# Kernel optimization log

Hardware: AMD Instinct MI355X
Metric: run time of the kernel (lower is better)

Reference implementation:

```python
import jax, jax.numpy as jnp
import numpy as np

N = 10000
E = 320000
IN_DIM = 512

def spmm(vals, row, col, x):
    # adj @ x with adjacency given as COO edge list: sum_e vals[e] * x[col[e]] into row[e]
    return jax.ops.segment_sum(vals[:, None] * x[col], row, num_segments=N)

def setup_inputs() -> dict:
    key = jax.random.key(0)
    ks = jax.random.split(key, 12)
    inp = {
        'features': jax.random.normal(ks[0], (N, IN_DIM), dtype=jnp.float32),
        'adj_row': jax.random.randint(ks[1], (E,), 0, N, dtype=jnp.int32),
        'adj_col': jax.random.randint(ks[2], (E,), 0, N, dtype=jnp.int32),
        'adj_vals': jax.random.uniform(ks[3], (E,), dtype=jnp.float32),
        'W0': jax.random.normal(ks[4], (IN_DIM, 32), dtype=jnp.float32) * 0.05,
        'W1': jax.random.normal(ks[5], (32, 32), dtype=jnp.float32) * 0.1,
        'W2': jax.random.normal(ks[6], (32, 32), dtype=jnp.float32) * 0.1,
        'W3': jax.random.normal(ks[7], (32, 32), dtype=jnp.float32) * 0.1,
        'W4': jax.random.normal(ks[8], (32, 32), dtype=jnp.float32) * 0.1,
        'W5': jax.random.normal(ks[9], (32, 32), dtype=jnp.float32) * 0.1,
        'W6': jax.random.normal(ks[10], (32, 16), dtype=jnp.float32) * 0.1,
    }
    return inp

def reference(features, adj_row, adj_col, adj_vals, W0, W1, W2, W3, W4, W5, W6):
    # GraphConvolutionSparse: (dropout omitted, rate=0) -> x@W -> adj@x -> relu
    h = jax.nn.relu(spmm(adj_vals, adj_row, adj_col, features @ W0))
    # 5 hidden GraphConvolution layers 32->32 with relu
    for W in (W1, W2, W3, W4, W5):
        h = jax.nn.relu(spmm(adj_vals, adj_row, adj_col, h @ W))
    # z_mean: linear activation, 32->16
    z = spmm(adj_vals, adj_row, adj_col, h @ W6)
    # InnerProductDecoder: flatten(z @ z.T), identity activation
    recon = (z @ z.T).reshape(-1)  # [N*N]
    return recon
```

## Files before the change

### kernel.cpp

```cpp
#include <hip/hip_runtime.h>

#define THREADS 256
#define CAP 128

typedef float floatx4 __attribute__((ext_vector_type(4)));


__global__ void zero_kernel(int* __restrict__ p, int n) {
    int i = blockIdx.x * blockDim.x + threadIdx.x;
    if (i < n) p[i] = 0;
}


__global__ void build_and_gemm0_kernel(const int* __restrict__ row, const int* __restrict__ col,
                                       const float* __restrict__ val, int* __restrict__ nxt,
                                       int* __restrict__ ell_c, float* __restrict__ ell_v, int E,
                                       const float* __restrict__ X, const float* __restrict__ W0,
                                       float* __restrict__ Y, int n, int K, int gridE) {
    if ((int)blockIdx.x < gridE) {
        int e = blockIdx.x * THREADS + threadIdx.x;
        if (e < E) {
            int r = row[e];
            int p = atomicAdd(&nxt[r], 1);
            if (p < CAP) {
                ell_c[r * CAP + p] = col[e];
                ell_v[r * CAP + p] = val[e];
            }
        }
    } else {
        int idx = (blockIdx.x - gridE) * THREADS + threadIdx.x;
        int r = idx >> 5;
        int f = idx & 31;
        if (r >= n) return;
        const float* xr = X + (size_t)r * K;
        float acc = 0.f;
        for (int k = 0; k < K; k += 4) {
            floatx4 x = *reinterpret_cast<const floatx4*>(xr + k);
            acc = fmaf(x.x, W0[(k + 0) * 32 + f], acc);
            acc = fmaf(x.y, W0[(k + 1) * 32 + f], acc);
            acc = fmaf(x.z, W0[(k + 2) * 32 + f], acc);
            acc = fmaf(x.w, W0[(k + 3) * 32 + f], acc);
        }
        Y[r * 32 + f] = acc;
    }
}


template <int FOUT>
__global__ void fused_spmm_gemm_kernel(const int* __restrict__ nxt, const int* __restrict__ ell_c,
                                       const float* __restrict__ ell_v, const float* __restrict__ Yin,
                                       const float* __restrict__ W, float* __restrict__ Yout, int n) {
    __shared__ float w[32 * FOUT];
    const int t = threadIdx.x;
    for (int i = t; i < 32 * FOUT; i += THREADS) w[i] = W[i];
    __syncthreads();

    int g = (blockIdx.x * THREADS + t) >> 5;
    if (g >= n) return;
    int f = t & 31;
    int deg = min(nxt[g], CAP);
    int base = g * CAP;
    float acc = 0.f;
    int i = 0;
    for (; i + 4 <= deg; i += 4) {
        int4   cc = *reinterpret_cast<const int4*>(ell_c + base + i);
        floatx4 vv = *reinterpret_cast<const floatx4*>(ell_v + base + i);
        float y0 = Yin[(size_t)cc.x * 32 + f];
        float y1 = Yin[(size_t)cc.y * 32 + f];
        float y2 = Yin[(size_t)cc.z * 32 + f];
        float y3 = Yin[(size_t)cc.w * 32 + f];
        acc = fmaf(vv.x, y0, acc);
        acc = fmaf(vv.y, y1, acc);
        acc = fmaf(vv.z, y2, acc);
        acc = fmaf(vv.w, y3, acc);
    }
    for (; i < deg; ++i)
        acc = fmaf(ell_v[base + i], Yin[(size_t)ell_c[base + i] * 32 + f], acc);
    float h = fmaxf(acc, 0.f);

    const int fo = f & (FOUT - 1);
    float y = 0.f;
#pragma unroll
    for (int k = 0; k < 32; ++k)
        y = fmaf(__shfl(h, k, 32), w[k * FOUT + fo], y);
    if (f < FOUT) Yout[(size_t)g * FOUT + f] = y;
}

__global__ void spmm16_kernel(const int* __restrict__ nxt, const int* __restrict__ ell_c,
                              const float* __restrict__ ell_v, const float* __restrict__ Yin,
                              float* __restrict__ Z, int n) {
    int g = (blockIdx.x * THREADS + threadIdx.x) >> 4;
    if (g >= n) return;
    int f = threadIdx.x & 15;
    int deg = min(nxt[g], CAP);
    int base = g * CAP;
    float acc = 0.f;
    int i = 0;
    for (; i + 4 <= deg; i += 4) {
        int4   cc = *reinterpret_cast<const int4*>(ell_c + base + i);
        floatx4 vv = *reinterpret_cast<const floatx4*>(ell_v + base + i);
        float y0 = Yin[(size_t)cc.x * 16 + f];
        float y1 = Yin[(size_t)cc.y * 16 + f];
        float y2 = Yin[(size_t)cc.z * 16 + f];
        float y3 = Yin[(size_t)cc.w * 16 + f];
        acc = fmaf(vv.x, y0, acc);
        acc = fmaf(vv.y, y1, acc);
        acc = fmaf(vv.z, y2, acc);
        acc = fmaf(vv.w, y3, acc);
    }
    for (; i < deg; ++i)
        acc = fmaf(ell_v[base + i], Yin[(size_t)ell_c[base + i] * 16 + f], acc);
    Z[(size_t)g * 16 + f] = acc;
}


__global__ void zzt_kernel(const float* __restrict__ z, float* __restrict__ out, int n) {
    __shared__ float zi[32][16];
    const int t = threadIdx.x;
    const int bi = blockIdx.y * 32;
    for (int i = t; i < 512; i += THREADS) {
        int r = i >> 4, c = i & 15;
        zi[r][c] = (bi + r < n) ? z[(size_t)(bi + r) * 16 + c] : 0.f;
    }
    __syncthreads();
    int j0 = blockIdx.x * 1024 + t * 4;
    if (j0 >= n) return;
    float zj[4][16];
#pragma unroll
    for (int jj = 0; jj < 4; ++jj) {
#pragma unroll
        for (int k = 0; k < 16; k += 4) {
            floatx4 v = *reinterpret_cast<const floatx4*>(z + (size_t)(j0 + jj) * 16 + k);
            zj[jj][k] = v.x; zj[jj][k + 1] = v.y; zj[jj][k + 2] = v.z; zj[jj][k + 3] = v.w;
        }
    }
#pragma unroll 4
    for (int i = 0; i < 32; ++i) {
        if (bi + i >= n) break;
        floatx4 o = {0.f, 0.f, 0.f, 0.f};
#pragma unroll
        for (int k = 0; k < 16; ++k) {
            float a = zi[i][k];
            o.x = fmaf(a, zj[0][k], o.x);
            o.y = fmaf(a, zj[1][k], o.y);
            o.z = fmaf(a, zj[2][k], o.z);
            o.w = fmaf(a, zj[3][k], o.w);
        }
        __builtin_nontemporal_store(o, reinterpret_cast<floatx4*>(out + (size_t)(bi + i) * n + j0));
    }
}


extern "C" void kernel_launch(void* const* d_in, const int* in_sizes, int n_in,
                              void* d_out, int out_size, void* d_ws, size_t ws_size,
                              hipStream_t stream) {
    const float* features = (const float*)d_in[0];
    const int*   adj_row  = (const int*)d_in[1];
    const int*   adj_col  = (const int*)d_in[2];
    const float* adj_vals = (const float*)d_in[3];
    const float* W0 = (const float*)d_in[4];
    const float* Wh[5] = {(const float*)d_in[5], (const float*)d_in[6], (const float*)d_in[7],
                          (const float*)d_in[8], (const float*)d_in[9]};
    const float* W6 = (const float*)d_in[10];

    const int E = in_sizes[1];
    const int K = in_sizes[4] / 32;
    const int N = in_sizes[0] / K;

    char* ws = (char*)d_ws;
    size_t off = 0;
    auto alloc = [&](size_t bytes) -> void* {
        void* p = ws + off;
        off = (off + bytes + 255) & ~(size_t)255;
        return p;
    };
    int*   nxt   = (int*)alloc((size_t)N * 4);
    int*   ell_c = (int*)alloc((size_t)N * CAP * 4);
    float* ell_v = (float*)alloc((size_t)N * CAP * 4);
    float* Ya    = (float*)alloc((size_t)N * 32 * 4);
    float* Yb    = (float*)alloc((size_t)N * 32 * 4);
    float* Y16   = (float*)alloc((size_t)N * 16 * 4);
    float* zbuf  = (float*)alloc((size_t)N * 16 * 4);

    const int gridE = (E + THREADS - 1) / THREADS;
    const int gridG = (N * 32 + THREADS - 1) / THREADS;
    const int gridRow = gridG;

    zero_kernel<<<(N + THREADS - 1) / THREADS, THREADS, 0, stream>>>(nxt, N);
    build_and_gemm0_kernel<<<gridE + gridG, THREADS, 0, stream>>>(
        adj_row, adj_col, adj_vals, nxt, ell_c, ell_v, E, features, W0, Ya, N, K, gridE);

    float* yin = Ya;
    float* yout = Yb;
    for (int l = 0; l < 5; ++l) {
        fused_spmm_gemm_kernel<32><<<gridRow, THREADS, 0, stream>>>(nxt, ell_c, ell_v, yin, Wh[l], yout, N);
        float* tmp = yin; yin = yout; yout = tmp;
    }
    fused_spmm_gemm_kernel<16><<<gridRow, THREADS, 0, stream>>>(nxt, ell_c, ell_v, yin, W6, Y16, N);
    spmm16_kernel<<<(N * 16 + THREADS - 1) / THREADS, THREADS, 0, stream>>>(nxt, ell_c, ell_v, Y16, zbuf, N);

    dim3 zg((N + 1023) / 1024, (N + 31) / 32);
    zzt_kernel<<<zg, THREADS, 0, stream>>>(zbuf, (float*)d_out, N);
}
```

Measured before the change: 249.6 us.

## Fuse GCN front layers into one cooperative persistent kernel with grid syncs

Replaces the chain of zero, build/GEMM0, six fused SpMM+GEMM and SpMM16 launches with a single cooperative kernel of 256 blocks of 1024 threads that uses grid.sync between stages. The aim is to remove per-kernel launch gaps and tail effects across the small dependent layers. The ZZ^T kernel still runs separately afterwards, and the old multi-kernel path remains as a fallback if the cooperative launch fails. The trade-offs are the cost of each grid-wide barrier and a fixed occupancy of one large block per CU.

```diff
diff --git a/kernel.cpp b/kernel.cpp
--- a/kernel.cpp
+++ b/kernel.cpp
@@ -1,16 +1,202 @@
 #include <hip/hip_runtime.h>
+#include <hip/hip_cooperative_groups.h>
+
+namespace cg = cooperative_groups;
 
 #define THREADS 256
+#define CTHREADS 1024
+#define CBLOCKS 256
 #define CAP 128
 
 typedef float floatx4 __attribute__((ext_vector_type(4)));
+
+
+__global__ __launch_bounds__(CTHREADS, 1) void front_kernel(
+    const int* __restrict__ adj_row, const int* __restrict__ adj_col, const float* __restrict__ adj_val,
+    const float* __restrict__ X,
+    const float* __restrict__ W0, const float* __restrict__ W1, const float* __restrict__ W2,
+    const float* __restrict__ W3, const float* __restrict__ W4, const float* __restrict__ W5,
+    const float* __restrict__ W6,
+    int* __restrict__ nxt, int* __restrict__ ell_c, float* __restrict__ ell_v,
+    float* __restrict__ Ya, float* __restrict__ Yb, float* __restrict__ Y16, float* __restrict__ z,
+    int N, int E, int K)
+{
+    cg::grid_group grid = cg::this_grid();
+    __shared__ float w[32 * 32];
+    const int t = threadIdx.x;
+    const int gtid = blockIdx.x * CTHREADS + t;
+    const int NT = CBLOCKS * CTHREADS;
+
+    for (int i = gtid; i < N; i += NT) nxt[i] = 0;
+    grid.sync();
+
+    for (int e = gtid; e < E; e += NT) {
+        int r = adj_row[e];
+        int p = atomicAdd(&nxt[r], 1);
+        if (p < CAP) {
+            ell_c[r * CAP + p] = adj_col[e];
+            ell_v[r * CAP + p] = adj_val[e];
+        }
+    }
+    for (int idx = gtid; idx < N * 32; idx += NT) {
+        int r = idx >> 5, f = idx & 31;
+        const float* xr = X + (size_t)r * K;
+        float acc = 0.f;
+        for (int k = 0; k < K; k += 4) {
+            floatx4 x = *reinterpret_cast<const floatx4*>(xr + k);
+            acc = fmaf(x.x, W0[(k + 0) * 32 + f], acc);
+            acc = fmaf(x.y, W0[(k + 1) * 32 + f], acc);
+            acc = fmaf(x.z, W0[(k + 2) * 32 + f], acc);
+            acc = fmaf(x.w, W0[(k + 3) * 32 + f], acc);
+        }
+        Ya[idx] = acc;
+    }
+    grid.sync();
+
+    const int group = gtid >> 5;
+    const int NG = NT >> 5;
+    const int f = t & 31;
+
+    const float* Wl[5] = {W1, W2, W3, W4, W5};
+    float* yin = Ya;
+    float* yout = Yb;
+#pragma unroll
+    for (int l = 0; l < 5; ++l) {
+        __syncthreads();
+        for (int i = t; i < 32 * 32; i += CTHREADS) w[i] = Wl[l][i];
+        __syncthreads();
+        for (int r = group; r < N; r += NG) {
+            int deg = min(nxt[r], CAP);
+            int base = r * CAP;
+            float acc = 0.f;
+            int i = 0;
+            for (; i + 4 <= deg; i += 4) {
+                int4    cc = *reinterpret_cast<const int4*>(ell_c + base + i);
+                floatx4 vv = *reinterpret_cast<const floatx4*>(ell_v + base + i);
+                float y0 = yin[(size_t)cc.x * 32 + f];
+                float y1 = yin[(size_t)cc.y * 32 + f];
+                float y2 = yin[(size_t)cc.z * 32 + f];
+                float y3 = yin[(size_t)cc.w * 32 + f];
+                acc = fmaf(vv.x, y0, acc);
+                acc = fmaf(vv.y, y1, acc);
+                acc = fmaf(vv.z, y2, acc);
+                acc = fmaf(vv.w, y3, acc);
+            }
+            for (; i < deg; ++i)
+                acc = fmaf(ell_v[base + i], yin[(size_t)ell_c[base + i] * 32 + f], acc);
+            float h = fmaxf(acc, 0.f);
+            float y = 0.f;
+#pragma unroll
+            for (int k = 0; k < 32; ++k)
+                y = fmaf(__shfl(h, k, 32), w[k * 32 + f], y);
+            yout[r * 32 + f] = y;
+        }
+        grid.sync();
+        float* tmp = yin; yin = yout; yout = tmp;
+    }
+
+    __syncthreads();
+    for (int i = t; i < 32 * 16; i += CTHREADS) w[i] = W6[i];
+    __syncthreads();
+    for (int r = group; r < N; r += NG) {
+        int deg = min(nxt[r], CAP);
+        int base = r * CAP;
+        float acc = 0.f;
+        int i = 0;
+        for (; i + 4 <= deg; i += 4) {
+            int4    cc = *reinterpret_cast<const int4*>(ell_c + base + i);
+            floatx4 vv = *reinterpret_cast<const floatx4*>(ell_v + base + i);
+            float y0 = yin[(size_t)cc.x * 32 + f];
+            float y1 = yin[(size_t)cc.y * 32 + f];
+            float y2 = yin[(size_t)cc.z * 32 + f];
+            float y3 = yin[(size_t)cc.w * 32 + f];
+            acc = fmaf(vv.x, y0, acc);
+            acc = fmaf(vv.y, y1, acc);
+            acc = fmaf(vv.z, y2, acc);
+            acc = fmaf(vv.w, y3, acc);
+        }
+        for (; i < deg; ++i)
+            acc = fmaf(ell_v[base + i], yin[(size_t)ell_c[base + i] * 32 + f], acc);
+        float h = fmaxf(acc, 0.f);
+        int fo = f & 15;
+        float y = 0.f;
+#pragma unroll
+        for (int k = 0; k < 32; ++k)
+            y = fmaf(__shfl(h, k, 32), w[k * 16 + fo], y);
+        if (f < 16) Y16[r * 16 + fo] = y;
+    }
+    grid.sync();
+
+    {
+        const int group16 = gtid >> 4;
+        const int NG16 = NT >> 4;
+        const int ff = t & 15;
+        for (int r = group16; r < N; r += NG16) {
+            int deg = min(nxt[r], CAP);
+            int base = r * CAP;
+            float acc = 0.f;
+            int i = 0;
+            for (; i + 4 <= deg; i += 4) {
+                int4    cc = *reinterpret_cast<const int4*>(ell_c + base + i);
+                floatx4 vv = *reinterpret_cast<const floatx4*>(ell_v + base + i);
+                float y0 = Y16[(size_t)cc.x * 16 + ff];
+                float y1 = Y16[(size_t)cc.y * 16 + ff];
+                float y2 = Y16[(size_t)cc.z * 16 + ff];
+                float y3 = Y16[(size_t)cc.w * 16 + ff];
+                acc = fmaf(vv.x, y0, acc);
+                acc = fmaf(vv.y, y1, acc);
+                acc = fmaf(vv.z, y2, acc);
+                acc = fmaf(vv.w, y3, acc);
+            }
+            for (; i < deg; ++i)
+                acc = fmaf(ell_v[base + i], Y16[(size_t)ell_c[base + i] * 16 + ff], acc);
+            z[(size_t)r * 16 + ff] = acc;
+        }
+    }
+}
+
+
+__global__ void zzt_kernel(const float* __restrict__ z, float* __restrict__ out, int n) {
+    __shared__ float zi[32][16];
+    const int t = threadIdx.x;
+    const int bi = blockIdx.y * 32;
+    for (int i = t; i < 512; i += THREADS) {
+        int r = i >> 4, c = i & 15;
+        zi[r][c] = (bi + r < n) ? z[(size_t)(bi + r) * 16 + c] : 0.f;
+    }
+    __syncthreads();
+    int j0 = blockIdx.x * 1024 + t * 4;
+    if (j0 >= n) return;
+    float zj[4][16];
+#pragma unroll
+    for (int jj = 0; jj < 4; ++jj) {
+#pragma unroll
+        for (int k = 0; k < 16; k += 4) {
+            floatx4 v = *reinterpret_cast<const floatx4*>(z + (size_t)(j0 + jj) * 16 + k);
+            zj[jj][k] = v.x; zj[jj][k + 1] = v.y; zj[jj][k + 2] = v.z; zj[jj][k + 3] = v.w;
+        }
+    }
+#pragma unroll 4
+    for (int i = 0; i < 32; ++i) {
+        if (bi + i >= n) break;
+        floatx4 o = {0.f, 0.f, 0.f, 0.f};
+#pragma unroll
+        for (int k = 0; k < 16; ++k) {
+            float a = zi[i][k];
+            o.x = fmaf(a, zj[0][k], o.x);
+            o.y = fmaf(a, zj[1][k], o.y);
+            o.z = fmaf(a, zj[2][k], o.z);
+            o.w = fmaf(a, zj[3][k], o.w);
+        }
+        __builtin_nontemporal_store(o, reinterpret_cast<floatx4*>(out + (size_t)(bi + i) * n + j0));
+    }
+}
 
 
 __global__ void zero_kernel(int* __restrict__ p, int n) {
     int i = blockIdx.x * blockDim.x + threadIdx.x;
     if (i < n) p[i] = 0;
 }
-
 
 __global__ void build_and_gemm0_kernel(const int* __restrict__ row, const int* __restrict__ col,
                                        const float* __restrict__ val, int* __restrict__ nxt,
@@ -45,7 +231,6 @@
     }
 }
 
-
 template <int FOUT>
 __global__ void fused_spmm_gemm_kernel(const int* __restrict__ nxt, const int* __restrict__ ell_c,
                                        const float* __restrict__ ell_v, const float* __restrict__ Yin,
@@ -63,7 +248,7 @@
     float acc = 0.f;
     int i = 0;
     for (; i + 4 <= deg; i += 4) {
-        int4   cc = *reinterpret_cast<const int4*>(ell_c + base + i);
+        int4    cc = *reinterpret_cast<const int4*>(ell_c + base + i);
         floatx4 vv = *reinterpret_cast<const floatx4*>(ell_v + base + i);
         float y0 = Yin[(size_t)cc.x * 32 + f];
         float y1 = Yin[(size_t)cc.y * 32 + f];
@@ -97,7 +282,7 @@
     float acc = 0.f;
     int i = 0;
     for (; i + 4 <= deg; i += 4) {
-        int4   cc = *reinterpret_cast<const int4*>(ell_c + base + i);
+        int4    cc = *reinterpret_cast<const int4*>(ell_c + base + i);
         floatx4 vv = *reinterpret_cast<const floatx4*>(ell_v + base + i);
         float y0 = Yin[(size_t)cc.x * 16 + f];
         float y1 = Yin[(size_t)cc.y * 16 + f];
@@ -114,43 +299,6 @@
 }
 
 
-__global__ void zzt_kernel(const float* __restrict__ z, float* __restrict__ out, int n) {
-    __shared__ float zi[32][16];
-    const int t = threadIdx.x;
-    const int bi = blockIdx.y * 32;
-    for (int i = t; i < 512; i += THREADS) {
-        int r = i >> 4, c = i & 15;
-        zi[r][c] = (bi + r < n) ? z[(size_t)(bi + r) * 16 + c] : 0.f;
-    }
-    __syncthreads();
-    int j0 = blockIdx.x * 1024 + t * 4;
-    if (j0 >= n) return;
-    float zj[4][16];
-#pragma unroll
-    for (int jj = 0; jj < 4; ++jj) {
-#pragma unroll
-        for (int k = 0; k < 16; k += 4) {
-            floatx4 v = *reinterpret_cast<const floatx4*>(z + (size_t)(j0 + jj) * 16 + k);
-            zj[jj][k] = v.x; zj[jj][k + 1] = v.y; zj[jj][k + 2] = v.z; zj[jj][k + 3] = v.w;
-        }
-    }
-#pragma unroll 4
-    for (int i = 0; i < 32; ++i) {
-        if (bi + i >= n) break;
-        floatx4 o = {0.f, 0.f, 0.f, 0.f};
-#pragma unroll
-        for (int k = 0; k < 16; ++k) {
-            float a = zi[i][k];
-            o.x = fmaf(a, zj[0][k], o.x);
-            o.y = fmaf(a, zj[1][k], o.y);
-            o.z = fmaf(a, zj[2][k], o.z);
-            o.w = fmaf(a, zj[3][k], o.w);
-        }
-        __builtin_nontemporal_store(o, reinterpret_cast<floatx4*>(out + (size_t)(bi + i) * n + j0));
-    }
-}
-
-
 extern "C" void kernel_launch(void* const* d_in, const int* in_sizes, int n_in,
                               void* d_out, int out_size, void* d_ws, size_t ws_size,
                               hipStream_t stream) {
@@ -159,13 +307,16 @@
     const int*   adj_col  = (const int*)d_in[2];
     const float* adj_vals = (const float*)d_in[3];
     const float* W0 = (const float*)d_in[4];
-    const float* Wh[5] = {(const float*)d_in[5], (const float*)d_in[6], (const float*)d_in[7],
-                          (const float*)d_in[8], (const float*)d_in[9]};
+    const float* W1 = (const float*)d_in[5];
+    const float* W2 = (const float*)d_in[6];
+    const float* W3 = (const float*)d_in[7];
+    const float* W4 = (const float*)d_in[8];
+    const float* W5 = (const float*)d_in[9];
     const float* W6 = (const float*)d_in[10];
 
-    const int E = in_sizes[1];
-    const int K = in_sizes[4] / 32;
-    const int N = in_sizes[0] / K;
+    int E = in_sizes[1];
+    int K = in_sizes[4] / 32;
+    int N = in_sizes[0] / K;
 
     char* ws = (char*)d_ws;
     size_t off = 0;
@@ -182,6 +333,23 @@
     float* Y16   = (float*)alloc((size_t)N * 16 * 4);
     float* zbuf  = (float*)alloc((size_t)N * 16 * 4);
 
+    float* out = (float*)d_out;
+    dim3 zg((N + 1023) / 1024, (N + 31) / 32);
+
+    void* args[] = {
+        (void*)&adj_row, (void*)&adj_col, (void*)&adj_vals, (void*)&features,
+        (void*)&W0, (void*)&W1, (void*)&W2, (void*)&W3, (void*)&W4, (void*)&W5, (void*)&W6,
+        (void*)&nxt, (void*)&ell_c, (void*)&ell_v,
+        (void*)&Ya, (void*)&Yb, (void*)&Y16, (void*)&zbuf,
+        (void*)&N, (void*)&E, (void*)&K,
+    };
+    hipError_t err = hipLaunchCooperativeKernel((void*)front_kernel, dim3(CBLOCKS), dim3(CTHREADS),
+                                                args, 0, stream);
+    if (err == hipSuccess) {
+        zzt_kernel<<<zg, THREADS, 0, stream>>>(zbuf, out, N);
+        return;
+    }
+
     const int gridE = (E + THREADS - 1) / THREADS;
     const int gridG = (N * 32 + THREADS - 1) / THREADS;
     const int gridRow = gridG;
@@ -190,6 +358,7 @@
     build_and_gemm0_kernel<<<gridE + gridG, THREADS, 0, stream>>>(
         adj_row, adj_col, adj_vals, nxt, ell_c, ell_v, E, features, W0, Ya, N, K, gridE);
 
+    const float* Wh[5] = {W1, W2, W3, W4, W5};
     float* yin = Ya;
     float* yout = Yb;
     for (int l = 0; l < 5; ++l) {
@@ -199,6 +368,5 @@
     fused_spmm_gemm_kernel<16><<<gridRow, THREADS, 0, stream>>>(nxt, ell_c, ell_v, yin, W6, Y16, N);
     spmm16_kernel<<<(N * 16 + THREADS - 1) / THREADS, THREADS, 0, stream>>>(nxt, ell_c, ell_v, Y16, zbuf, N);
 
-    dim3 zg((N + 1023) / 1024, (N + 31) / 32);
-    zzt_kernel<<<zg, THREADS, 0, stream>>>(zbuf, (float*)d_out, N);
-}
+    zzt_kernel<<<zg, THREADS, 0, stream>>>(zbuf, out, N);
+}
```

New measurement: 493.5 us. 97.7% more time.
